# Optimization experiments

Measured on AMD Instinct MI355X. Metric: run time of the kernel, lower is better.

## Reference

```python
import jax, jax.numpy as jnp
import numpy as np

H = 16
DH = 64


def setup_inputs() -> dict:
    key = jax.random.key(0)
    ks = jax.random.split(key, 8)
    b, n, m, d = 2, 2048, 2048, 1024
    inner = H * DH  # 1024
    return {
        "x": jax.random.normal(ks[0], (b, n, d), jnp.float32),
        "mem_k": jax.random.normal(ks[1], (b, m, inner), jnp.float32),
        "mem_v": jax.random.normal(ks[2], (b, m, inner), jnp.float32),
        "Wq": jax.random.normal(ks[3], (d, inner), jnp.float32) * (d ** -0.5),
        "Wkv": jax.random.normal(ks[4], (d, 2 * inner), jnp.float32) * (d ** -0.5),
        "b_kv": jax.random.normal(ks[5], (2 * inner,), jnp.float32) * 0.02,
        "Wo": jax.random.normal(ks[6], (inner, d), jnp.float32) * (inner ** -0.5),
        "b_o": jax.random.normal(ks[7], (d,), jnp.float32) * 0.02,
    }


def reference(x, mem_k, mem_v, Wq, Wkv, b_kv, Wo, b_o):
    b, n, d = x.shape
    scale = DH ** -0.5
    q = (x @ Wq) * scale                       # [b, n, h*dh]
    self_k, self_v = jnp.split(x @ Wkv + b_kv, 2, axis=-1)
    k = jnp.concatenate([mem_k, self_k], axis=1)   # [b, j, h*dh]
    v = jnp.concatenate([mem_v, self_v], axis=1)

    def split_heads(t):
        return t.reshape(b, t.shape[1], H, DH).transpose(0, 2, 1, 3)  # b h n d

    q, k, v = map(split_heads, (q, k, v))
    sim = jnp.einsum('bhid,bhjd->bhij', q, k)  # [b, h, n, j]
    i, j = sim.shape[-2:]
    # causal mask: query i may attend to keys up to position (j - i) + i
    causal_mask = jnp.triu(jnp.ones((i, j), dtype=bool), k=j - i + 1)
    mask_value = -jnp.finfo(sim.dtype).max
    sim = jnp.where(causal_mask[None, None], mask_value, sim)
    attn = jax.nn.softmax(sim, axis=-1)
    out = jnp.einsum('bhij,bhjd->bhid', attn, v)
    out = out.transpose(0, 2, 1, 3).reshape(b, n, H * DH)
    return out @ Wo + b_o
```

## Files before the change

kernel.cpp:

```cpp
#include <hip/hip_runtime.h>
#include <stdint.h>

typedef __bf16 bf16x8 __attribute__((ext_vector_type(8)));
typedef _Float16 f16x8 __attribute__((ext_vector_type(8)));
typedef float f32x4 __attribute__((ext_vector_type(4)));

constexpr int Mm = 2048;
constexpr float QSCALE = 0.18033688011112042f;

__device__ __forceinline__ float exp2_fast(float x) {
  return __builtin_amdgcn_exp2f(x);
}

__device__ __forceinline__ uint16_t f2bf(float f) {
  union { float f; uint32_t u; } v; v.f = f;
  return (uint16_t)((v.u + 0x7FFFu + ((v.u >> 16) & 1u)) >> 16);
}
__device__ __forceinline__ uint32_t pack2(float a, float b) {
  return (uint32_t)f2bf(a) | ((uint32_t)f2bf(b) << 16);
}
__device__ __forceinline__ uint32_t pkrtz(float a, float b) {
  auto h2 = __builtin_amdgcn_cvt_pkrtz(a, b);
  return __builtin_bit_cast(uint32_t, h2);
}
__device__ __forceinline__ uint16_t f2h(float f) {
  _Float16 h = (_Float16)f;
  return __builtin_bit_cast(uint16_t, h);
}

__device__ __forceinline__ void async16(const void* g, void* l) {
  __builtin_amdgcn_global_load_lds(
      (__attribute__((address_space(1))) uint32_t*)g,
      (__attribute__((address_space(3))) uint32_t*)l, 16, 0, 0);
}

__device__ __forceinline__ bf16x8 frag64(const uint16_t* base, int row, int chunk) {
  return *(const bf16x8*)(base + row * 64 + chunk * 8);
}
__device__ __forceinline__ f16x8 frag64h(const uint16_t* base, int row, int chunk) {
  return *(const f16x8*)(base + row * 64 + chunk * 8);
}

__global__ __launch_bounds__(256) void prep_kernel(
    const float* __restrict__ x, const float* __restrict__ mem_k,
    const float* __restrict__ mem_v, const float* __restrict__ Wq,
    const float* __restrict__ Wkv, const float* __restrict__ Wo,
    uint16_t* __restrict__ Xb, uint16_t* __restrict__ WallT,
    uint16_t* __restrict__ WoT, uint16_t* __restrict__ Kh,
    uint16_t* __restrict__ VhT) {
  __shared__ float tile[64][65];
  __shared__ uint16_t vtile[64 * 66];
  const int tid = threadIdx.x;
  int blk = blockIdx.x;

  if (blk < 1024) {
    const float4* x4 = (const float4*)x;
    for (int it = 0; it < 4; ++it) {
      int idx4 = blk * 1024 + it * 256 + tid;
      float4 v = x4[idx4];
      uint2 w; w.x = pack2(v.x, v.y); w.y = pack2(v.z, v.w);
      ((uint2*)Xb)[idx4] = w;
    }
    return;
  }
  blk -= 1024;
  if (blk < 1024) {
    const float* src; uint16_t* dst; int ld, colbase, n0, k0;
    if (blk < 768) {
      int nt = blk >> 4, kt = blk & 15;
      n0 = nt * 64; k0 = kt * 64;
      if (n0 < 1024) { src = Wq; ld = 1024; colbase = n0; }
      else           { src = Wkv; ld = 2048; colbase = n0 - 1024; }
      dst = WallT;
    } else {
      int b2 = blk - 768;
      int nt = b2 >> 4, kt = b2 & 15;
      n0 = nt * 64; k0 = kt * 64;
      src = Wo; ld = 1024; colbase = n0; dst = WoT;
    }
    int r = tid >> 4, c = (tid & 15) * 4;
    for (int it = 0; it < 4; ++it) {
      int rr = r + it * 16;
      float4 v = *(const float4*)(src + (size_t)(k0 + rr) * ld + colbase + c);
      tile[rr][c] = v.x; tile[rr][c + 1] = v.y;
      tile[rr][c + 2] = v.z; tile[rr][c + 3] = v.w;
    }
    __syncthreads();
    for (int it = 0; it < 4; ++it) {
      int rn = r + it * 16;
      uint2 w;
      w.x = pack2(tile[c][rn], tile[c + 1][rn]);
      w.y = pack2(tile[c + 2][rn], tile[c + 3][rn]);
      *(uint2*)(dst + (size_t)(n0 + rn) * 1024 + k0 + c) = w;
    }
    return;
  }
  blk -= 1024;
  if (blk < 1024) {
    const float4* s4 = (const float4*)mem_k;
    for (int it = 0; it < 4; ++it) {
      int idx4 = blk * 1024 + it * 256 + tid;
      int e = idx4 * 4;
      int b = e >> 21;
      int rem = e & ((1 << 21) - 1);
      int m = rem >> 10;
      int cc = rem & 1023;
      int h = cc >> 6, dh = cc & 63;
      float4 v = s4[idx4];
      uint2 w; w.x = pack2(v.x, v.y); w.y = pack2(v.z, v.w);
      *(uint2*)(Kh + (((size_t)(b * 16 + h) * 4096) + m) * 64 + dh) = w;
    }
    return;
  }
  blk -= 1024;
  {
    const int b = blk >> 9, h = (blk >> 5) & 15, m0 = (blk & 31) * 64;
    const float4* s4 = (const float4*)mem_v;
    for (int it = 0; it < 4; ++it) {
      int idx = it * 256 + tid;
      int r = idx >> 4, d4 = (idx & 15) * 4;
      float4 v = s4[(size_t)(b * 2048 + m0 + r) * 256 + h * 16 + (d4 >> 2)];
      *(uint32_t*)&vtile[r * 66 + d4]     = pkrtz(v.x, v.y);
      *(uint32_t*)&vtile[r * 66 + d4 + 2] = pkrtz(v.z, v.w);
    }
    __syncthreads();
    int d = tid & 63;
    for (int half = 0; half < 2; ++half) {
      int mg = (tid >> 6) + half * 4;
      uint32_t w[4];
      for (int p = 0; p < 4; ++p) {
        uint32_t lo = vtile[(mg * 8 + 2 * p) * 66 + d];
        uint32_t hi = vtile[(mg * 8 + 2 * p + 1) * 66 + d];
        w[p] = lo | (hi << 16);
      }
      *(uint4*)&VhT[((size_t)((b * 16 + h) * 64) + d) * 4096 + m0 + mg * 8] =
          *(uint4*)w;
    }
  }
}

template <int MODE>
__global__ __launch_bounds__(256) void gemm_kernel(
    const uint16_t* __restrict__ A, const uint16_t* __restrict__ Bt,
    const float* __restrict__ bias, uint16_t* __restrict__ Qh,
    uint16_t* __restrict__ Kh, uint16_t* __restrict__ VhT,
    float* __restrict__ Out) {
  constexpr int K = 1024;
  constexpr int SS = 136;
  const int m0 = blockIdx.x * 128, n0 = blockIdx.y * 128;
  const int tid = threadIdx.x;
  const int wave = tid >> 6, lane = tid & 63;
  const int lhi = lane >> 4, llo = lane & 15;
  const int wm = (wave >> 1) * 64, wn = (wave & 1) * 64;

  __shared__ uint16_t sh[MODE == 0 ? 128 * SS : 128 * 128];
  uint16_t* As = sh;
  uint16_t* Bs = sh + 128 * 64;

  f32x4 acc[4][4] = {};

  for (int kt = 0; kt < K / 64; ++kt) {
    __syncthreads();
    for (int c = 0; c < 4; ++c) {
      int cl = (wave * 4 + c) * 64 + lane;
      int row = cl >> 3;
      int ch = cl & 7;
      async16(A + (size_t)(m0 + row) * K + kt * 64 + ch * 8, As + cl * 8);
      async16(Bt + (size_t)(n0 + row) * K + kt * 64 + ch * 8, Bs + cl * 8);
    }
    __syncthreads();
    for (int ks = 0; ks < 2; ++ks) {
      bf16x8 af[4], bfr[4];
      for (int mt = 0; mt < 4; ++mt) af[mt] = frag64(As, wm + mt * 16 + llo, ks * 4 + lhi);
      for (int nt = 0; nt < 4; ++nt) bfr[nt] = frag64(Bs, wn + nt * 16 + llo, ks * 4 + lhi);
      for (int mt = 0; mt < 4; ++mt)
        for (int nt = 0; nt < 4; ++nt)
          acc[mt][nt] = __builtin_amdgcn_mfma_f32_16x16x32_bf16(af[mt], bfr[nt], acc[mt][nt], 0, 0, 0);
    }
  }

  if (MODE == 0) {
    const int region = n0 >> 10;
    __syncthreads();
    for (int nt = 0; nt < 4; ++nt) {
      int cloc = wn + nt * 16 + llo;
      int col = n0 + cloc;
      float badd = (region == 0) ? 0.f : bias[col - 1024];
      for (int mt = 0; mt < 4; ++mt) {
        int rloc = wm + mt * 16 + lhi * 4;
        for (int reg = 0; reg < 4; ++reg) {
          float v = acc[mt][nt][reg];
          v = (region == 0) ? v * QSCALE : v + badd;
          if (region == 2) sh[cloc * SS + rloc + reg] = f2h(v);
          else             sh[(rloc + reg) * SS + cloc] = f2bf(v);
        }
      }
    }
    __syncthreads();
    if (region == 2) {
      const int rl = (tid & 15) * 8;
      for (int it = 0; it < 8; ++it) {
        int cloc = (tid >> 4) + it * 16;
        int col = n0 + cloc;
        int cc = col - 2048, h = cc >> 6, dh = cc & 63;
        int r = m0 + rl;
        int b = r >> 11, n = r & 2047;
        uint4 w = *(const uint4*)&sh[cloc * SS + rl];
        *(uint4*)&VhT[((size_t)((b * 16 + h) * 64) + dh) * 4096 + 2048 + n] = w;
      }
    } else {
      const int cl16 = (tid & 15) * 8;
      const int col = n0 + cl16;
      for (int it = 0; it < 8; ++it) {
        int rloc = (tid >> 4) + it * 16;
        int r = m0 + rloc;
        int b = r >> 11, n = r & 2047;
        uint4 w = *(const uint4*)&sh[rloc * SS + cl16];
        if (region == 0) {
          int h = col >> 6, dh = col & 63;
          *(uint4*)&Qh[(((size_t)(b * 16 + h) * 2048) + n) * 64 + dh] = w;
        } else {
          int cc = col - 1024, h = cc >> 6, dh = cc & 63;
          *(uint4*)&Kh[(((size_t)(b * 16 + h) * 4096) + 2048 + n) * 64 + dh] = w;
        }
      }
    }
  } else {
    for (int nt = 0; nt < 4; ++nt) {
      int col = n0 + wn + nt * 16 + llo;
      float bo = bias[col];
      for (int mt = 0; mt < 4; ++mt) {
        int rbase = m0 + wm + mt * 16 + lhi * 4;
        for (int reg = 0; reg < 4; ++reg)
          Out[(size_t)(rbase + reg) * 1024 + col] = acc[mt][nt][reg] + bo;
      }
    }
  }
}

__global__ __launch_bounds__(256, 2) void attn_kernel(
    const uint16_t* __restrict__ Qh, const uint16_t* __restrict__ Kh,
    const uint16_t* __restrict__ VhT, uint16_t* __restrict__ AO) {
  const int bh = blockIdx.x;
  const int qt = 15 - blockIdx.y;
  const int tid = threadIdx.x;
  const int wave = tid >> 6, lane = tid & 63;
  const int lhi = lane >> 4, llo = lane & 15;
  const int i0 = qt * 128;

  __shared__ uint16_t Ks[2][64 * 64];
  __shared__ uint16_t Vt[2][64 * 64];
  __shared__ uint16_t Ps[4][2][16 * 64];

  bf16x8 qf[2][2];
  for (int g = 0; g < 2; ++g) {
    const uint16_t* Qw =
        Qh + ((size_t)bh * 2048 + i0 + wave * 32 + g * 16 + llo) * 64;
    qf[g][0] = *(const bf16x8*)(Qw + lhi * 8);
    qf[g][1] = *(const bf16x8*)(Qw + 32 + lhi * 8);
  }

  const uint16_t* Kbh = Kh + (size_t)bh * 4096 * 64;
  const uint16_t* Vbh = VhT + (size_t)bh * 64 * 4096;

  f16x8 onesf;
  for (int i = 0; i < 8; ++i) onesf[i] = (_Float16)1.0f;

  f32x4 o[2][4] = {};
  f32x4 o4[2] = {};

  const int nkt = 34 + 2 * qt;
  const int swz = llo & 7;

  auto stage = [&](int buf, int t) {
    const int k0 = t * 64;
    for (int c = 0; c < 2; ++c) {
      int cl = (wave * 2 + c) * 64 + lane;
      int row = cl >> 3, ch = cl & 7;
      int chs = ch ^ (row & 7);
      async16(Kbh + (size_t)(k0 + row) * 64 + chs * 8, &Ks[buf][cl * 8]);
      async16(Vbh + (size_t)row * 4096 + k0 + chs * 8, &Vt[buf][cl * 8]);
    }
  };

  stage(0, 0);

  for (int t = 0; t < nkt; ++t) {
    const int cur = t & 1;
    const int k0 = t * 64;
    __syncthreads();
    if (t + 1 < nkt) stage(cur ^ 1, t + 1);

    f32x4 s[2][4] = {};
    for (int ks = 0; ks < 2; ++ks)
      for (int nt = 0; nt < 4; ++nt) {
        bf16x8 kf = frag64(&Ks[cur][0], nt * 16 + llo, (ks * 4 + lhi) ^ swz);
        s[0][nt] = __builtin_amdgcn_mfma_f32_16x16x32_bf16(kf, qf[0][ks], s[0][nt], 0, 0, 0);
        s[1][nt] = __builtin_amdgcn_mfma_f32_16x16x32_bf16(kf, qf[1][ks], s[1][nt], 0, 0, 0);
      }

    for (int g = 0; g < 2; ++g) {
      const int iw = i0 + wave * 32 + g * 16;
      if (k0 + 63 > Mm + iw) {
        int lim = Mm + iw + llo;
        for (int nt = 0; nt < 4; ++nt)
          for (int reg = 0; reg < 4; ++reg) {
            int j = k0 + nt * 16 + lhi * 4 + reg;
            if (j > lim) s[g][nt][reg] = -INFINITY;
          }
      }
      uint16_t* pw = &Ps[wave][g][0];
      for (int nt = 0; nt < 4; ++nt) {
        float p0 = exp2_fast(s[g][nt][0]);
        float p1 = exp2_fast(s[g][nt][1]);
        float p2 = exp2_fast(s[g][nt][2]);
        float p3 = exp2_fast(s[g][nt][3]);
        uint2 w; w.x = pkrtz(p0, p1); w.y = pkrtz(p2, p3);
        int c8 = 2 * nt + (lhi >> 1);
        *(uint2*)(pw + llo * 64 + (c8 ^ swz) * 8 + (lhi & 1) * 4) = w;
      }
    }

    for (int ks = 0; ks < 2; ++ks) {
      f16x8 pa0 = *(const f16x8*)(&Ps[wave][0][0] + llo * 64 + ((4 * ks + lhi) ^ swz) * 8);
      f16x8 pa1 = *(const f16x8*)(&Ps[wave][1][0] + llo * 64 + ((4 * ks + lhi) ^ swz) * 8);
      for (int nt = 0; nt < 4; ++nt) {
        f16x8 vf = frag64h(&Vt[cur][0], nt * 16 + llo, (ks * 4 + lhi) ^ swz);
        o[0][nt] = __builtin_amdgcn_mfma_f32_16x16x32_f16(pa0, vf, o[0][nt], 0, 0, 0);
        o[1][nt] = __builtin_amdgcn_mfma_f32_16x16x32_f16(pa1, vf, o[1][nt], 0, 0, 0);
      }
      o4[0] = __builtin_amdgcn_mfma_f32_16x16x32_f16(pa0, onesf, o4[0], 0, 0, 0);
      o4[1] = __builtin_amdgcn_mfma_f32_16x16x32_f16(pa1, onesf, o4[1], 0, 0, 0);
    }
  }

  const int b = bh >> 4, h = bh & 15;
  uint16_t* Es = &Ks[0][0];
  __syncthreads();
  for (int g = 0; g < 2; ++g) {
    float inv[4];
    for (int reg = 0; reg < 4; ++reg) inv[reg] = 1.0f / o4[g][reg];
    for (int nt = 0; nt < 4; ++nt)
      for (int reg = 0; reg < 4; ++reg)
        Es[(wave * 32 + g * 16 + lhi * 4 + reg) * 64 + nt * 16 + llo] =
            f2bf(o[g][nt][reg] * inv[reg]);
  }
  __syncthreads();
  {
    int row = tid >> 1, c32 = (tid & 1) * 32;
    size_t base = ((size_t)(b * 2048) + i0 + row) * 1024 + h * 64 + c32;
    *(uint4*)&AO[base]      = *(const uint4*)&Es[row * 64 + c32];
    *(uint4*)&AO[base + 8]  = *(const uint4*)&Es[row * 64 + c32 + 8];
    *(uint4*)&AO[base + 16] = *(const uint4*)&Es[row * 64 + c32 + 16];
    *(uint4*)&AO[base + 24] = *(const uint4*)&Es[row * 64 + c32 + 24];
  }
}

extern "C" void kernel_launch(void* const* d_in, const int* in_sizes, int n_in,
                              void* d_out, int out_size, void* d_ws,
                              size_t ws_size, hipStream_t stream) {
  const float* x     = (const float*)d_in[0];
  const float* mem_k = (const float*)d_in[1];
  const float* mem_v = (const float*)d_in[2];
  const float* Wq    = (const float*)d_in[3];
  const float* Wkv   = (const float*)d_in[4];
  const float* b_kv  = (const float*)d_in[5];
  const float* Wo    = (const float*)d_in[6];
  const float* b_o   = (const float*)d_in[7];
  float* out = (float*)d_out;

  char* ws = (char*)d_ws;
  uint16_t* Xb    = (uint16_t*)(ws);
  uint16_t* WallT = (uint16_t*)(ws + (8ull << 20));
  uint16_t* WoT   = (uint16_t*)(ws + (14ull << 20));
  uint16_t* Qh    = (uint16_t*)(ws + (16ull << 20));
  uint16_t* Kh    = (uint16_t*)(ws + (24ull << 20));
  uint16_t* VhT   = (uint16_t*)(ws + (40ull << 20));
  uint16_t* AO    = (uint16_t*)(ws + (56ull << 20));

  prep_kernel<<<4096, 256, 0, stream>>>(x, mem_k, mem_v, Wq, Wkv, Wo,
                                        Xb, WallT, WoT, Kh, VhT);
  gemm_kernel<0><<<dim3(32, 24), 256, 0, stream>>>(Xb, WallT, b_kv,
                                                   Qh, Kh, VhT, nullptr);
  attn_kernel<<<dim3(32, 16), 256, 0, stream>>>(Qh, Kh, VhT, AO);
  gemm_kernel<1><<<dim3(32, 8), 256, 0, stream>>>(AO, WoT, b_o,
                                                  nullptr, nullptr, nullptr, out);
}
```

Baseline: 267.6 us.

## Switch attention to 32x32 MFMA with in-register P via permlane32 swap

Rewrites the attention inner loop to use 32x32x16 MFMA instructions instead of 16x16x32, so each wave handles its 32 query rows as a single tile. The probability tile is now rearranged in registers with v_permlane32_swap instead of a round trip through per-wave LDS, which removes the Ps shared buffer and its stores and loads. It also adds s_setprio around the MFMA groups to favour matrix issue. The risks are a different register footprint from the 16-float accumulators and a new, more intricate fragment layout to get right.

```diff
diff --git a/kernel.cpp b/kernel.cpp
--- a/kernel.cpp
+++ b/kernel.cpp
@@ -4,6 +4,7 @@
 typedef __bf16 bf16x8 __attribute__((ext_vector_type(8)));
 typedef _Float16 f16x8 __attribute__((ext_vector_type(8)));
 typedef float f32x4 __attribute__((ext_vector_type(4)));
+typedef float f32x16 __attribute__((ext_vector_type(16)));
 
 constexpr int Mm = 2048;
 constexpr float QSCALE = 0.18033688011112042f;
@@ -245,32 +246,33 @@
   const int qt = 15 - blockIdx.y;
   const int tid = threadIdx.x;
   const int wave = tid >> 6, lane = tid & 63;
-  const int lhi = lane >> 4, llo = lane & 15;
+  const int lo5 = lane & 31, hi = lane >> 5;
   const int i0 = qt * 128;
+  const int iw = i0 + wave * 32;
+  const int swz5 = lo5 & 7;
 
   __shared__ uint16_t Ks[2][64 * 64];
   __shared__ uint16_t Vt[2][64 * 64];
-  __shared__ uint16_t Ps[4][2][16 * 64];
-
-  bf16x8 qf[2][2];
-  for (int g = 0; g < 2; ++g) {
-    const uint16_t* Qw =
-        Qh + ((size_t)bh * 2048 + i0 + wave * 32 + g * 16 + llo) * 64;
-    qf[g][0] = *(const bf16x8*)(Qw + lhi * 8);
-    qf[g][1] = *(const bf16x8*)(Qw + 32 + lhi * 8);
+
+  bf16x8 qf[4];
+  {
+    const uint16_t* Qw = Qh + ((size_t)bh * 2048 + iw + lo5) * 64;
+#pragma unroll
+    for (int kstep = 0; kstep < 4; ++kstep)
+      qf[kstep] = *(const bf16x8*)(Qw + kstep * 16 + hi * 8);
   }
 
   const uint16_t* Kbh = Kh + (size_t)bh * 4096 * 64;
   const uint16_t* Vbh = VhT + (size_t)bh * 64 * 4096;
 
   f16x8 onesf;
+#pragma unroll
   for (int i = 0; i < 8; ++i) onesf[i] = (_Float16)1.0f;
 
-  f32x4 o[2][4] = {};
-  f32x4 o4[2] = {};
+  f32x16 o0 = {}, o1 = {};
+  f32x16 lacc = {};
 
   const int nkt = 34 + 2 * qt;
-  const int swz = llo & 7;
 
   auto stage = [&](int buf, int t) {
     const int k0 = t * 64;
@@ -291,59 +293,62 @@
     __syncthreads();
     if (t + 1 < nkt) stage(cur ^ 1, t + 1);
 
-    f32x4 s[2][4] = {};
-    for (int ks = 0; ks < 2; ++ks)
-      for (int nt = 0; nt < 4; ++nt) {
-        bf16x8 kf = frag64(&Ks[cur][0], nt * 16 + llo, (ks * 4 + lhi) ^ swz);
-        s[0][nt] = __builtin_amdgcn_mfma_f32_16x16x32_bf16(kf, qf[0][ks], s[0][nt], 0, 0, 0);
-        s[1][nt] = __builtin_amdgcn_mfma_f32_16x16x32_bf16(kf, qf[1][ks], s[1][nt], 0, 0, 0);
-      }
-
-    for (int g = 0; g < 2; ++g) {
-      const int iw = i0 + wave * 32 + g * 16;
-      if (k0 + 63 > Mm + iw) {
-        int lim = Mm + iw + llo;
-        for (int nt = 0; nt < 4; ++nt)
-          for (int reg = 0; reg < 4; ++reg) {
-            int j = k0 + nt * 16 + lhi * 4 + reg;
-            if (j > lim) s[g][nt][reg] = -INFINITY;
-          }
-      }
-      uint16_t* pw = &Ps[wave][g][0];
-      for (int nt = 0; nt < 4; ++nt) {
-        float p0 = exp2_fast(s[g][nt][0]);
-        float p1 = exp2_fast(s[g][nt][1]);
-        float p2 = exp2_fast(s[g][nt][2]);
-        float p3 = exp2_fast(s[g][nt][3]);
-        uint2 w; w.x = pkrtz(p0, p1); w.y = pkrtz(p2, p3);
-        int c8 = 2 * nt + (lhi >> 1);
-        *(uint2*)(pw + llo * 64 + (c8 ^ swz) * 8 + (lhi & 1) * 4) = w;
-      }
-    }
-
-    for (int ks = 0; ks < 2; ++ks) {
-      f16x8 pa0 = *(const f16x8*)(&Ps[wave][0][0] + llo * 64 + ((4 * ks + lhi) ^ swz) * 8);
-      f16x8 pa1 = *(const f16x8*)(&Ps[wave][1][0] + llo * 64 + ((4 * ks + lhi) ^ swz) * 8);
-      for (int nt = 0; nt < 4; ++nt) {
-        f16x8 vf = frag64h(&Vt[cur][0], nt * 16 + llo, (ks * 4 + lhi) ^ swz);
-        o[0][nt] = __builtin_amdgcn_mfma_f32_16x16x32_f16(pa0, vf, o[0][nt], 0, 0, 0);
-        o[1][nt] = __builtin_amdgcn_mfma_f32_16x16x32_f16(pa1, vf, o[1][nt], 0, 0, 0);
-      }
-      o4[0] = __builtin_amdgcn_mfma_f32_16x16x32_f16(pa0, onesf, o4[0], 0, 0, 0);
-      o4[1] = __builtin_amdgcn_mfma_f32_16x16x32_f16(pa1, onesf, o4[1], 0, 0, 0);
+#pragma unroll
+    for (int mblk = 0; mblk < 2; ++mblk) {
+      f32x16 s = {};
+      __builtin_amdgcn_s_setprio(1);
+#pragma unroll
+      for (int kstep = 0; kstep < 4; ++kstep) {
+        bf16x8 kf = frag64(&Ks[cur][0], mblk * 32 + lo5, (2 * kstep + hi) ^ swz5);
+        s = __builtin_amdgcn_mfma_f32_32x32x16_bf16(kf, qf[kstep], s, 0, 0, 0);
+      }
+      __builtin_amdgcn_s_setprio(0);
+
+      if (k0 + mblk * 32 + 31 > Mm + iw) {
+        const int lim = Mm + iw + lo5 - k0 - mblk * 32;
+#pragma unroll
+        for (int r = 0; r < 16; ++r) {
+          int kl = (r & 3) + 8 * (r >> 2) + 4 * hi;
+          if (kl > lim) s[r] = -INFINITY;
+        }
+      }
+
+      uint32_t c[8];
+#pragma unroll
+      for (int w = 0; w < 8; ++w)
+        c[w] = pkrtz(exp2_fast(s[2 * w]), exp2_fast(s[2 * w + 1]));
+
+#pragma unroll
+      for (int kk2 = 0; kk2 < 2; ++kk2) {
+        uint32_t w0 = c[4 * kk2 + 0], w2 = c[4 * kk2 + 2];
+        uint32_t w1 = c[4 * kk2 + 1], w3 = c[4 * kk2 + 3];
+        asm volatile("v_permlane32_swap_b32 %0, %1" : "+v"(w0), "+v"(w2));
+        asm volatile("v_permlane32_swap_b32 %0, %1" : "+v"(w1), "+v"(w3));
+        uint4 fw; fw.x = w0; fw.y = w1; fw.z = w2; fw.w = w3;
+        f16x8 pa = __builtin_bit_cast(f16x8, fw);
+        const int kk = mblk * 2 + kk2;
+        __builtin_amdgcn_s_setprio(1);
+        {
+          f16x8 vf0 = frag64h(&Vt[cur][0], lo5,      (2 * kk + hi) ^ swz5);
+          f16x8 vf1 = frag64h(&Vt[cur][0], 32 + lo5, (2 * kk + hi) ^ swz5);
+          o0 = __builtin_amdgcn_mfma_f32_32x32x16_f16(pa, vf0, o0, 0, 0, 0);
+          o1 = __builtin_amdgcn_mfma_f32_32x32x16_f16(pa, vf1, o1, 0, 0, 0);
+          lacc = __builtin_amdgcn_mfma_f32_32x32x16_f16(pa, onesf, lacc, 0, 0, 0);
+        }
+        __builtin_amdgcn_s_setprio(0);
+      }
     }
   }
 
   const int b = bh >> 4, h = bh & 15;
   uint16_t* Es = &Ks[0][0];
   __syncthreads();
-  for (int g = 0; g < 2; ++g) {
-    float inv[4];
-    for (int reg = 0; reg < 4; ++reg) inv[reg] = 1.0f / o4[g][reg];
-    for (int nt = 0; nt < 4; ++nt)
-      for (int reg = 0; reg < 4; ++reg)
-        Es[(wave * 32 + g * 16 + lhi * 4 + reg) * 64 + nt * 16 + llo] =
-            f2bf(o[g][nt][reg] * inv[reg]);
+#pragma unroll
+  for (int r = 0; r < 16; ++r) {
+    float inv = 1.0f / lacc[r];
+    int q = wave * 32 + (r & 3) + 8 * (r >> 2) + 4 * hi;
+    Es[q * 64 + lo5]      = f2bf(o0[r] * inv);
+    Es[q * 64 + 32 + lo5] = f2bf(o1[r] * inv);
   }
   __syncthreads();
   {
```

Result: no change. 264.5 us (-1.2%).
